# Kernel tuning notes

Hardware: AMD Instinct MI355X
Metric: run time of the kernel (lower is better)

Reference implementation:

```python
import jax, jax.numpy as jnp
import numpy as np

N_NODES = 100000


def gcn_conv(x, edge_index, W, b, num_nodes):
    """PyG GCNConv: y = D^{-1/2} (A + I) D^{-1/2} (x W) + b.

    edge_index[0] = source (row), edge_index[1] = target (col);
    messages flow source -> target with symmetric normalization.
    """
    # add self loops
    loop = jnp.arange(num_nodes, dtype=edge_index.dtype)
    row = jnp.concatenate([edge_index[0], loop])  # [E+N]
    col = jnp.concatenate([edge_index[1], loop])  # [E+N]

    xw = x @ W  # [N, F_out] -- tiny GEMM, done before gather

    # degree of target nodes (incl. self loops)
    ones = jnp.ones(col.shape[0], dtype=x.dtype)
    deg = jax.ops.segment_sum(ones, col, num_segments=num_nodes)  # [N]
    dis = jax.lax.rsqrt(jnp.maximum(deg, 1e-12))
    dis = jnp.where(deg > 0, dis, 0.0)

    norm = dis[row] * dis[col]  # [E+N]
    msg = xw[row] * norm[:, None]  # gather + scale, [E+N, F_out]
    out = jax.ops.segment_sum(msg, col, num_segments=num_nodes)  # scatter-add
    return out + b


def setup_inputs() -> dict:
    key = jax.random.key(0)
    k1, k2, k3, k4 = jax.random.split(key, 4)
    num_attr, hidden, num_classes = 128, 16, 8
    n_edges = 3200000
    x = jax.random.normal(k1, (N_NODES, num_attr), dtype=jnp.float32)
    edge_index = jax.random.randint(k2, (2, n_edges), 0, N_NODES, dtype=jnp.int64)
    W1 = jax.random.normal(k3, (num_attr, hidden), dtype=jnp.float32) / np.sqrt(num_attr)
    b1 = jnp.zeros((hidden,), dtype=jnp.float32)
    W2 = jax.random.normal(k4, (hidden, num_classes), dtype=jnp.float32) / np.sqrt(hidden)
    b2 = jnp.zeros((num_classes,), dtype=jnp.float32)
    return {"x": x, "edge_index": edge_index, "W1": W1, "b1": b1, "W2": W2, "b2": b2}


def reference(x, edge_index, W1, b1, W2, b2):
    h = gcn_conv(x, edge_index, W1, b1, N_NODES)
    h = jax.nn.relu(h)
    # dropout is identity in eval mode
    h = gcn_conv(h, edge_index, W2, b2, N_NODES)
    return jax.nn.sigmoid(h)  # [N, num_classes]
```

## Files before the change

### kernel.cpp

```cpp
#include <hip/hip_runtime.h>
#include <math.h>

static constexpr int FI = 128;
static constexpr int FH = 16;
static constexpr int FO = 8;

static constexpr int BIN_SHIFT = 8;
static constexpr int BIN_NODES = 256;
static constexpr int MAX_BINS  = 512;
static constexpr int CAPB      = 8832;
static constexpr int SCHUNK    = 8192;
static constexpr int SThreads  = 512;

__device__ __forceinline__ unsigned short f2bf(float x) {
    unsigned u = __float_as_uint(x);
    u += 0x7FFFu + ((u >> 16) & 1u);
    return (unsigned short)(u >> 16);
}
__device__ __forceinline__ float bflo(unsigned u) { return __uint_as_float(u << 16); }
__device__ __forceinline__ float bfhi(unsigned u) { return __uint_as_float(u & 0xFFFF0000u); }

__global__ void k_initcur(int* __restrict__ binCursor, int nbins) {
    int i = blockIdx.x * 256 + threadIdx.x;
    if (i < nbins) binCursor[i] = i * CAPB;
}

__launch_bounds__(SThreads)
__global__ void k_binscatter(const int* __restrict__ row, const int* __restrict__ col,
                             int* __restrict__ binCursor, unsigned int* __restrict__ binned,
                             int E, int nbins) {
    __shared__ int lcnt[MAX_BINS];
    __shared__ int lsc[MAX_BINS];
    __shared__ int lstart[MAX_BINS];
    __shared__ int lcur[MAX_BINS];
    __shared__ int gbase[MAX_BINS];
    __shared__ unsigned int   staged[SCHUNK];
    __shared__ unsigned short sbin[SCHUNK];
    int t = threadIdx.x;
    int base = blockIdx.x * SCHUNK;
    int end  = base + SCHUNK; if (end > E) end = E;
    int m = end - base;
    if (t < MAX_BINS) lcnt[t] = 0;
    __syncthreads();

    int nv = m >> 2;
    const int4* c4 = (const int4*)(col + base);
    for (int k = t; k < nv; k += SThreads) {
        int4 c = c4[k];
        atomicAdd(&lcnt[c.x >> BIN_SHIFT], 1);
        atomicAdd(&lcnt[c.y >> BIN_SHIFT], 1);
        atomicAdd(&lcnt[c.z >> BIN_SHIFT], 1);
        atomicAdd(&lcnt[c.w >> BIN_SHIFT], 1);
    }
    for (int i = base + (nv << 2) + t; i < end; i += SThreads)
        atomicAdd(&lcnt[col[i] >> BIN_SHIFT], 1);
    __syncthreads();

    int v = 0;
    if (t < MAX_BINS) { v = lcnt[t]; lsc[t] = v; }
    __syncthreads();
    for (int off = 1; off < MAX_BINS; off <<= 1) {
        int x = (t >= off && t < MAX_BINS) ? lsc[t - off] : 0;
        __syncthreads();
        if (t < MAX_BINS) lsc[t] += x;
        __syncthreads();
    }
    if (t < MAX_BINS) {
        int ex = lsc[t] - v;
        lstart[t] = ex;
        lcur[t]   = ex;
        gbase[t]  = v ? atomicAdd(&binCursor[t], v) : 0;
    }
    __syncthreads();

    const int4* r4 = (const int4*)(row + base);
    for (int k = t; k < nv; k += SThreads) {
        int4 c = c4[k]; int4 r = r4[k];
        int cc[4] = {c.x, c.y, c.z, c.w};
        int rr[4] = {r.x, r.y, r.z, r.w};
        #pragma unroll
        for (int j = 0; j < 4; ++j) {
            int b = cc[j] >> BIN_SHIFT;
            int pos = atomicAdd(&lcur[b], 1);
            staged[pos] = (unsigned)rr[j] | ((unsigned)(cc[j] & (BIN_NODES - 1)) << 17);
            sbin[pos] = (unsigned short)b;
        }
    }
    for (int i = base + (nv << 2) + t; i < end; i += SThreads) {
        int c = col[i];
        int b = c >> BIN_SHIFT;
        int pos = atomicAdd(&lcur[b], 1);
        staged[pos] = (unsigned)row[i] | ((unsigned)(c & (BIN_NODES - 1)) << 17);
        sbin[pos] = (unsigned short)b;
    }
    __syncthreads();

    for (int i = t; i < m; i += SThreads) {
        int b = sbin[i];
        int g = gbase[b] + (i - lstart[b]);
        if (g < (b + 1) * CAPB) binned[g] = staged[i];
    }
}

__launch_bounds__(BIN_NODES)
__global__ void k_refine(const int* __restrict__ binCursor, const unsigned int* __restrict__ binned,
                         int* __restrict__ srow, int* __restrict__ starts, int* __restrict__ ends,
                         float* __restrict__ dis, int N) {
    __shared__ int cnt[BIN_NODES];
    __shared__ int wsum[4];
    int t = threadIdx.x;
    int b = blockIdx.x;
    int s = b * CAPB;
    int m = binCursor[b] - s;
    if (m > CAPB) m = CAPB;
    cnt[t] = 0;
    __syncthreads();

    int mm = m & ~3;
    for (int i0 = t * 4; i0 < mm; i0 += BIN_NODES * 4) {
        uint4 v = *(const uint4*)(binned + s + i0);
        atomicAdd(&cnt[v.x >> 17], 1);
        atomicAdd(&cnt[v.y >> 17], 1);
        atomicAdd(&cnt[v.z >> 17], 1);
        atomicAdd(&cnt[v.w >> 17], 1);
    }
    for (int i = mm + t; i < m; i += BIN_NODES)
        atomicAdd(&cnt[binned[s + i] >> 17], 1);
    __syncthreads();

    int deg = cnt[t];
    int inc = deg;
    #pragma unroll
    for (int d = 1; d < 64; d <<= 1) {
        int u = __shfl_up(inc, d, 64);
        if ((t & 63) >= d) inc += u;
    }
    if ((t & 63) == 63) wsum[t >> 6] = inc;
    __syncthreads();
    if (t < 4) {
        int w = wsum[t];
        #pragma unroll
        for (int d = 1; d < 4; d <<= 1) {
            int u = __shfl_up(w, d, 4);
            if (t >= d) w += u;
        }
        wsum[t] = w;
    }
    __syncthreads();
    int waveoff = (t >= 64) ? wsum[(t >> 6) - 1] : 0;
    int excl = waveoff + inc - deg;

    int n = b * BIN_NODES + t;
    if (n < N) {
        starts[n] = s + excl;
        ends[n]   = s + excl + deg;
        dis[n]    = rsqrtf((float)(deg + 1));
    }
    cnt[t] = excl;
    __syncthreads();

    for (int i0 = t * 4; i0 < mm; i0 += BIN_NODES * 4) {
        uint4 v = *(const uint4*)(binned + s + i0);
        int p0 = atomicAdd(&cnt[v.x >> 17], 1); srow[s + p0] = v.x & 0x1FFFF;
        int p1 = atomicAdd(&cnt[v.y >> 17], 1); srow[s + p1] = v.y & 0x1FFFF;
        int p2 = atomicAdd(&cnt[v.z >> 17], 1); srow[s + p2] = v.z & 0x1FFFF;
        int p3 = atomicAdd(&cnt[v.w >> 17], 1); srow[s + p3] = v.w & 0x1FFFF;
    }
    for (int i = mm + t; i < m; i += BIN_NODES) {
        unsigned v = binned[s + i];
        int p = atomicAdd(&cnt[v >> 17], 1);
        srow[s + p] = v & 0x1FFFF;
    }
}

__launch_bounds__(256)
__global__ void k_gemm1(const float* __restrict__ x, const float* __restrict__ W,
                        const float* __restrict__ dis, unsigned short* __restrict__ xw1s,
                        int N) {
    __shared__ float sw[FI * FH];
    int t = threadIdx.x;
    for (int i = t; i < FI * FH; i += 256) sw[i] = W[i];
    __syncthreads();

    int nl = t >> 2;
    int f  = (t & 3) * 4;
    int n  = blockIdx.x * 64 + nl;
    if (n >= N) return;

    const float4* xr = (const float4*)(x + (size_t)n * FI);
    float a0 = 0.f, a1 = 0.f, a2 = 0.f, a3 = 0.f;
    #pragma unroll 8
    for (int kq = 0; kq < FI / 4; ++kq) {
        float4 xv = xr[kq];
        float4 w0 = *(const float4*)&sw[(kq * 4 + 0) * FH + f];
        float4 w1 = *(const float4*)&sw[(kq * 4 + 1) * FH + f];
        float4 w2 = *(const float4*)&sw[(kq * 4 + 2) * FH + f];
        float4 w3 = *(const float4*)&sw[(kq * 4 + 3) * FH + f];
        a0 = fmaf(xv.x, w0.x, a0); a1 = fmaf(xv.x, w0.y, a1);
        a2 = fmaf(xv.x, w0.z, a2); a3 = fmaf(xv.x, w0.w, a3);
        a0 = fmaf(xv.y, w1.x, a0); a1 = fmaf(xv.y, w1.y, a1);
        a2 = fmaf(xv.y, w1.z, a2); a3 = fmaf(xv.y, w1.w, a3);
        a0 = fmaf(xv.z, w2.x, a0); a1 = fmaf(xv.z, w2.y, a1);
        a2 = fmaf(xv.z, w2.z, a2); a3 = fmaf(xv.z, w2.w, a3);
        a0 = fmaf(xv.w, w3.x, a0); a1 = fmaf(xv.w, w3.y, a1);
        a2 = fmaf(xv.w, w3.z, a2); a3 = fmaf(xv.w, w3.w, a3);
    }
    float dn = dis[n];
    unsigned w0 = (unsigned)f2bf(a0 * dn) | ((unsigned)f2bf(a1 * dn) << 16);
    unsigned w1 = (unsigned)f2bf(a2 * dn) | ((unsigned)f2bf(a3 * dn) << 16);
    *(uint2*)(xw1s + (size_t)n * FH + f) = make_uint2(w0, w1);
}

__launch_bounds__(128)
__global__ void k_agg1(const int* __restrict__ starts, const int* __restrict__ ends,
                       const int* __restrict__ srow, const float* __restrict__ dis,
                       const unsigned short* __restrict__ xw1s, const float* __restrict__ W2,
                       const float* __restrict__ b1, unsigned short* __restrict__ xw2s, int N) {
    __shared__ float sw[FH * FO];
    __shared__ float sb[FH];
    int t = threadIdx.x;
    if (t < FH * FO) sw[t] = W2[t];
    if (t < FH) sb[t] = b1[t];
    __syncthreads();

    int n = blockIdx.x * 128 + t;
    if (n >= N) return;
    float dn = dis[n];
    int s = starts[n], e = ends[n];
    const uint4* xq = (const uint4*)xw1s;

    uint4 s0 = xq[(size_t)n * 2], s1 = xq[(size_t)n * 2 + 1];
    float acc[16];
    acc[0]=bflo(s0.x); acc[1]=bfhi(s0.x); acc[2]=bflo(s0.y); acc[3]=bfhi(s0.y);
    acc[4]=bflo(s0.z); acc[5]=bfhi(s0.z); acc[6]=bflo(s0.w); acc[7]=bfhi(s0.w);
    acc[8]=bflo(s1.x); acc[9]=bfhi(s1.x); acc[10]=bflo(s1.y); acc[11]=bfhi(s1.y);
    acc[12]=bflo(s1.z); acc[13]=bfhi(s1.z); acc[14]=bflo(s1.w); acc[15]=bfhi(s1.w);

    int i = s;
    for (; i + 8 <= e; i += 8) {
        int rr[8];
        #pragma unroll
        for (int j = 0; j < 8; ++j) rr[j] = srow[i + j];
        uint4 pa[8], pb[8];
        #pragma unroll
        for (int j = 0; j < 8; ++j) {
            pa[j] = xq[(size_t)rr[j] * 2];
            pb[j] = xq[(size_t)rr[j] * 2 + 1];
        }
        #pragma unroll
        for (int j = 0; j < 8; ++j) {
            acc[0]+=bflo(pa[j].x);  acc[1]+=bfhi(pa[j].x);
            acc[2]+=bflo(pa[j].y);  acc[3]+=bfhi(pa[j].y);
            acc[4]+=bflo(pa[j].z);  acc[5]+=bfhi(pa[j].z);
            acc[6]+=bflo(pa[j].w);  acc[7]+=bfhi(pa[j].w);
            acc[8]+=bflo(pb[j].x);  acc[9]+=bfhi(pb[j].x);
            acc[10]+=bflo(pb[j].y); acc[11]+=bfhi(pb[j].y);
            acc[12]+=bflo(pb[j].z); acc[13]+=bfhi(pb[j].z);
            acc[14]+=bflo(pb[j].w); acc[15]+=bfhi(pb[j].w);
        }
    }
    for (; i < e; ++i) {
        int r = srow[i];
        uint4 qa = xq[(size_t)r * 2], qb = xq[(size_t)r * 2 + 1];
        acc[0]+=bflo(qa.x);  acc[1]+=bfhi(qa.x);
        acc[2]+=bflo(qa.y);  acc[3]+=bfhi(qa.y);
        acc[4]+=bflo(qa.z);  acc[5]+=bfhi(qa.z);
        acc[6]+=bflo(qa.w);  acc[7]+=bfhi(qa.w);
        acc[8]+=bflo(qb.x);  acc[9]+=bfhi(qb.x);
        acc[10]+=bflo(qb.y); acc[11]+=bfhi(qb.y);
        acc[12]+=bflo(qb.z); acc[13]+=bfhi(qb.z);
        acc[14]+=bflo(qb.w); acc[15]+=bfhi(qb.w);
    }

    float hv[FH];
    #pragma unroll
    for (int k = 0; k < FH; ++k) {
        float v = fmaf(dn, acc[k], sb[k]);
        hv[k] = v > 0.f ? v : 0.f;
    }
    unsigned o[4];
    #pragma unroll
    for (int p = 0; p < 4; ++p) {
        float aL = 0.f, aH = 0.f;
        #pragma unroll
        for (int k = 0; k < FH; ++k) {
            aL = fmaf(hv[k], sw[k * FO + 2 * p],     aL);
            aH = fmaf(hv[k], sw[k * FO + 2 * p + 1], aH);
        }
        o[p] = (unsigned)f2bf(aL * dn) | ((unsigned)f2bf(aH * dn) << 16);
    }
    *(uint4*)(xw2s + (size_t)n * FO) = make_uint4(o[0], o[1], o[2], o[3]);
}

__launch_bounds__(128)
__global__ void k_agg2(const int* __restrict__ starts, const int* __restrict__ ends,
                       const int* __restrict__ srow, const float* __restrict__ dis,
                       const unsigned short* __restrict__ xw2s, const float* __restrict__ b2,
                       float* __restrict__ out, int N) {
    int t = threadIdx.x;
    int n = blockIdx.x * 128 + t;
    if (n >= N) return;
    float dn = dis[n];
    int s = starts[n], e = ends[n];
    const uint4* xq = (const uint4*)xw2s;

    uint4 sp = xq[n];
    float acc[8];
    acc[0]=bflo(sp.x); acc[1]=bfhi(sp.x); acc[2]=bflo(sp.y); acc[3]=bfhi(sp.y);
    acc[4]=bflo(sp.z); acc[5]=bfhi(sp.z); acc[6]=bflo(sp.w); acc[7]=bfhi(sp.w);

    int i = s;
    for (; i + 8 <= e; i += 8) {
        int rr[8];
        #pragma unroll
        for (int j = 0; j < 8; ++j) rr[j] = srow[i + j];
        uint4 pk[8];
        #pragma unroll
        for (int j = 0; j < 8; ++j) pk[j] = xq[rr[j]];
        #pragma unroll
        for (int j = 0; j < 8; ++j) {
            acc[0]+=bflo(pk[j].x); acc[1]+=bfhi(pk[j].x);
            acc[2]+=bflo(pk[j].y); acc[3]+=bfhi(pk[j].y);
            acc[4]+=bflo(pk[j].z); acc[5]+=bfhi(pk[j].z);
            acc[6]+=bflo(pk[j].w); acc[7]+=bfhi(pk[j].w);
        }
    }
    for (; i < e; ++i) {
        uint4 p = xq[srow[i]];
        acc[0]+=bflo(p.x); acc[1]+=bfhi(p.x);
        acc[2]+=bflo(p.y); acc[3]+=bfhi(p.y);
        acc[4]+=bflo(p.z); acc[5]+=bfhi(p.z);
        acc[6]+=bflo(p.w); acc[7]+=bfhi(p.w);
    }

    float r[FO];
    #pragma unroll
    for (int k = 0; k < FO; ++k) {
        float v = fmaf(dn, acc[k], b2[k]);
        r[k] = 1.f / (1.f + __expf(-v));
    }
    *(float4*)(out + (size_t)n * FO)     = make_float4(r[0], r[1], r[2], r[3]);
    *(float4*)(out + (size_t)n * FO + 4) = make_float4(r[4], r[5], r[6], r[7]);
}

extern "C" void kernel_launch(void* const* d_in, const int* in_sizes, int n_in,
                              void* d_out, int out_size, void* d_ws, size_t ws_size,
                              hipStream_t stream) {
    const float* x  = (const float*)d_in[0];
    const int*   ei = (const int*)d_in[1];
    const float* W1 = (const float*)d_in[2];
    const float* b1 = (const float*)d_in[3];
    const float* W2 = (const float*)d_in[4];
    const float* b2 = (const float*)d_in[5];

    const int N = in_sizes[0] / FI;
    const int E = in_sizes[1] / 2;
    const int* row = ei;
    const int* col = ei + E;
    const int nbins = (N + BIN_NODES - 1) >> BIN_SHIFT;

    const size_t NP = 100352;
    const size_t BINSZ = (size_t)nbins * CAPB;
    float* base = (float*)d_ws;
    int*   starts    = (int*)base;
    int*   ends      = (int*)(base + NP);
    float* dis       = base + 2 * NP;
    int*   binCursor = (int*)(base + 3 * NP);
    unsigned int* binned = (unsigned int*)(base + 3 * NP + 1024);
    int*   srow      = (int*)(base + 3 * NP + 1024 + BINSZ);
    unsigned short* xw1s = (unsigned short*)binned;
    unsigned short* xw2s = (unsigned short*)(base + 3 * NP + 1024 + NP * 8);
    float* out = (float*)d_out;

    size_t needed = (3 * NP + 1024 + 2 * BINSZ) * 4;
    if (ws_size < needed) return;

    k_initcur   <<<(nbins + 255) / 256, 256,             0, stream>>>(binCursor, nbins);
    k_binscatter<<<(E + SCHUNK - 1) / SCHUNK, SThreads,  0, stream>>>(row, col, binCursor, binned, E, nbins);
    k_refine    <<<nbins, BIN_NODES,                     0, stream>>>(binCursor, binned, srow, starts, ends, dis, N);
    k_gemm1     <<<(N + 63) / 64, 256,                   0, stream>>>(x, W1, dis, xw1s, N);
    k_agg1      <<<(N + 127) / 128, 128,                 0, stream>>>(starts, ends, srow, dis, xw1s, W2, b1, xw2s, N);
    k_agg2      <<<(N + 127) / 128, 128,                 0, stream>>>(starts, ends, srow, dis, xw2s, b2, out, N);
}
```

Measured before the change: 125.1 us.

## Fuse GEMM1 into refine kernel, split agg features across thread pairs, cache col in registers

```diff
diff --git a/kernel.cpp b/kernel.cpp
--- a/kernel.cpp
+++ b/kernel.cpp
@@ -45,12 +45,17 @@
 
     int nv = m >> 2;
     const int4* c4 = (const int4*)(col + base);
-    for (int k = t; k < nv; k += SThreads) {
-        int4 c = c4[k];
-        atomicAdd(&lcnt[c.x >> BIN_SHIFT], 1);
-        atomicAdd(&lcnt[c.y >> BIN_SHIFT], 1);
-        atomicAdd(&lcnt[c.z >> BIN_SHIFT], 1);
-        atomicAdd(&lcnt[c.w >> BIN_SHIFT], 1);
+    int4 creg[4];
+    #pragma unroll
+    for (int j = 0; j < 4; ++j) {
+        int k = t + j * SThreads;
+        if (k < nv) {
+            creg[j] = c4[k];
+            atomicAdd(&lcnt[creg[j].x >> BIN_SHIFT], 1);
+            atomicAdd(&lcnt[creg[j].y >> BIN_SHIFT], 1);
+            atomicAdd(&lcnt[creg[j].z >> BIN_SHIFT], 1);
+            atomicAdd(&lcnt[creg[j].w >> BIN_SHIFT], 1);
+        }
     }
     for (int i = base + (nv << 2) + t; i < end; i += SThreads)
         atomicAdd(&lcnt[col[i] >> BIN_SHIFT], 1);
@@ -74,16 +79,20 @@
     __syncthreads();
 
     const int4* r4 = (const int4*)(row + base);
-    for (int k = t; k < nv; k += SThreads) {
-        int4 c = c4[k]; int4 r = r4[k];
-        int cc[4] = {c.x, c.y, c.z, c.w};
-        int rr[4] = {r.x, r.y, r.z, r.w};
-        #pragma unroll
-        for (int j = 0; j < 4; ++j) {
-            int b = cc[j] >> BIN_SHIFT;
-            int pos = atomicAdd(&lcur[b], 1);
-            staged[pos] = (unsigned)rr[j] | ((unsigned)(cc[j] & (BIN_NODES - 1)) << 17);
-            sbin[pos] = (unsigned short)b;
+    #pragma unroll
+    for (int j = 0; j < 4; ++j) {
+        int k = t + j * SThreads;
+        if (k < nv) {
+            int4 r = r4[k];
+            int cc[4] = {creg[j].x, creg[j].y, creg[j].z, creg[j].w};
+            int rr[4] = {r.x, r.y, r.z, r.w};
+            #pragma unroll
+            for (int jj = 0; jj < 4; ++jj) {
+                int b = cc[jj] >> BIN_SHIFT;
+                int pos = atomicAdd(&lcur[b], 1);
+                staged[pos] = (unsigned)rr[jj] | ((unsigned)(cc[jj] & (BIN_NODES - 1)) << 17);
+                sbin[pos] = (unsigned short)b;
+            }
         }
     }
     for (int i = base + (nv << 2) + t; i < end; i += SThreads) {
@@ -102,18 +111,23 @@
     }
 }
 
-__launch_bounds__(BIN_NODES)
-__global__ void k_refine(const int* __restrict__ binCursor, const unsigned int* __restrict__ binned,
-                         int* __restrict__ srow, int* __restrict__ starts, int* __restrict__ ends,
-                         float* __restrict__ dis, int N) {
+__launch_bounds__(256)
+__global__ void k_refine_gemm(const int* __restrict__ binCursor, const unsigned int* __restrict__ binned,
+                              int* __restrict__ srow, int* __restrict__ starts, int* __restrict__ ends,
+                              float* __restrict__ dis, const float* __restrict__ x,
+                              const float* __restrict__ W1, unsigned short* __restrict__ xw1s, int N) {
     __shared__ int cnt[BIN_NODES];
     __shared__ int wsum[4];
+    __shared__ float sdis[BIN_NODES];
+    __shared__ float sw[FI * FH];
+    __shared__ float sx[64 * 132];
     int t = threadIdx.x;
     int b = blockIdx.x;
     int s = b * CAPB;
     int m = binCursor[b] - s;
     if (m > CAPB) m = CAPB;
     cnt[t] = 0;
+    for (int i = t; i < FI * FH; i += 256) sw[i] = W1[i];
     __syncthreads();
 
     int mm = m & ~3;
@@ -151,11 +165,13 @@
     int excl = waveoff + inc - deg;
 
     int n = b * BIN_NODES + t;
+    float dv = rsqrtf((float)(deg + 1));
     if (n < N) {
         starts[n] = s + excl;
         ends[n]   = s + excl + deg;
-        dis[n]    = rsqrtf((float)(deg + 1));
-    }
+        dis[n]    = dv;
+    }
+    sdis[t] = dv;
     cnt[t] = excl;
     __syncthreads();
 
@@ -171,47 +187,43 @@
         int p = atomicAdd(&cnt[v >> 17], 1);
         srow[s + p] = v & 0x1FFFF;
     }
-}
-
-__launch_bounds__(256)
-__global__ void k_gemm1(const float* __restrict__ x, const float* __restrict__ W,
-                        const float* __restrict__ dis, unsigned short* __restrict__ xw1s,
-                        int N) {
-    __shared__ float sw[FI * FH];
-    int t = threadIdx.x;
-    for (int i = t; i < FI * FH; i += 256) sw[i] = W[i];
-    __syncthreads();
 
     int nl = t >> 2;
     int f  = (t & 3) * 4;
-    int n  = blockIdx.x * 64 + nl;
-    if (n >= N) return;
-
-    const float4* xr = (const float4*)(x + (size_t)n * FI);
-    float a0 = 0.f, a1 = 0.f, a2 = 0.f, a3 = 0.f;
-    #pragma unroll 8
-    for (int kq = 0; kq < FI / 4; ++kq) {
-        float4 xv = xr[kq];
-        float4 w0 = *(const float4*)&sw[(kq * 4 + 0) * FH + f];
-        float4 w1 = *(const float4*)&sw[(kq * 4 + 1) * FH + f];
-        float4 w2 = *(const float4*)&sw[(kq * 4 + 2) * FH + f];
-        float4 w3 = *(const float4*)&sw[(kq * 4 + 3) * FH + f];
-        a0 = fmaf(xv.x, w0.x, a0); a1 = fmaf(xv.x, w0.y, a1);
-        a2 = fmaf(xv.x, w0.z, a2); a3 = fmaf(xv.x, w0.w, a3);
-        a0 = fmaf(xv.y, w1.x, a0); a1 = fmaf(xv.y, w1.y, a1);
-        a2 = fmaf(xv.y, w1.z, a2); a3 = fmaf(xv.y, w1.w, a3);
-        a0 = fmaf(xv.z, w2.x, a0); a1 = fmaf(xv.z, w2.y, a1);
-        a2 = fmaf(xv.z, w2.z, a2); a3 = fmaf(xv.z, w2.w, a3);
-        a0 = fmaf(xv.w, w3.x, a0); a1 = fmaf(xv.w, w3.y, a1);
-        a2 = fmaf(xv.w, w3.z, a2); a3 = fmaf(xv.w, w3.w, a3);
-    }
-    float dn = dis[n];
-    unsigned w0 = (unsigned)f2bf(a0 * dn) | ((unsigned)f2bf(a1 * dn) << 16);
-    unsigned w1 = (unsigned)f2bf(a2 * dn) | ((unsigned)f2bf(a3 * dn) << 16);
-    *(uint2*)(xw1s + (size_t)n * FH + f) = make_uint2(w0, w1);
-}
-
-__launch_bounds__(128)
+    for (int c = 0; c < 4; ++c) {
+        __syncthreads();
+        int rbase = b * BIN_NODES + c * 64;
+        int rows = N - rbase;
+        rows = rows < 0 ? 0 : (rows > 64 ? 64 : rows);
+        const float4* xg = (const float4*)(x + (size_t)rbase * FI);
+        for (int i = t; i < rows * 32; i += 256) {
+            int r = i >> 5, cc = i & 31;
+            float4 vv = xg[(size_t)r * 32 + cc];
+            float* dst = &sx[r * 132 + cc * 4];
+            dst[0] = vv.x; dst[1] = vv.y; dst[2] = vv.z; dst[3] = vv.w;
+        }
+        __syncthreads();
+        int nn = rbase + nl;
+        if (nn < N) {
+            float a0 = 0.f, a1 = 0.f, a2 = 0.f, a3 = 0.f;
+            #pragma unroll 4
+            for (int k = 0; k < FI; k++) {
+                float xv = sx[nl * 132 + k];
+                const float* wr = &sw[k * FH + f];
+                a0 = fmaf(xv, wr[0], a0);
+                a1 = fmaf(xv, wr[1], a1);
+                a2 = fmaf(xv, wr[2], a2);
+                a3 = fmaf(xv, wr[3], a3);
+            }
+            float dn = sdis[c * 64 + nl];
+            unsigned w0 = (unsigned)f2bf(a0 * dn) | ((unsigned)f2bf(a1 * dn) << 16);
+            unsigned w1 = (unsigned)f2bf(a2 * dn) | ((unsigned)f2bf(a3 * dn) << 16);
+            *(uint2*)(xw1s + (size_t)nn * FH + f) = make_uint2(w0, w1);
+        }
+    }
+}
+
+__launch_bounds__(256)
 __global__ void k_agg1(const int* __restrict__ starts, const int* __restrict__ ends,
                        const int* __restrict__ srow, const float* __restrict__ dis,
                        const unsigned short* __restrict__ xw1s, const float* __restrict__ W2,
@@ -223,124 +235,109 @@
     if (t < FH) sb[t] = b1[t];
     __syncthreads();
 
-    int n = blockIdx.x * 128 + t;
+    int n = blockIdx.x * 128 + (t >> 1);
+    int h = t & 1;
     if (n >= N) return;
     float dn = dis[n];
     int s = starts[n], e = ends[n];
     const uint4* xq = (const uint4*)xw1s;
 
-    uint4 s0 = xq[(size_t)n * 2], s1 = xq[(size_t)n * 2 + 1];
-    float acc[16];
-    acc[0]=bflo(s0.x); acc[1]=bfhi(s0.x); acc[2]=bflo(s0.y); acc[3]=bfhi(s0.y);
-    acc[4]=bflo(s0.z); acc[5]=bfhi(s0.z); acc[6]=bflo(s0.w); acc[7]=bfhi(s0.w);
-    acc[8]=bflo(s1.x); acc[9]=bfhi(s1.x); acc[10]=bflo(s1.y); acc[11]=bfhi(s1.y);
-    acc[12]=bflo(s1.z); acc[13]=bfhi(s1.z); acc[14]=bflo(s1.w); acc[15]=bfhi(s1.w);
+    uint4 sp = xq[(size_t)n * 2 + h];
+    float acc[8];
+    acc[0]=bflo(sp.x); acc[1]=bfhi(sp.x); acc[2]=bflo(sp.y); acc[3]=bfhi(sp.y);
+    acc[4]=bflo(sp.z); acc[5]=bfhi(sp.z); acc[6]=bflo(sp.w); acc[7]=bfhi(sp.w);
 
     int i = s;
     for (; i + 8 <= e; i += 8) {
         int rr[8];
         #pragma unroll
         for (int j = 0; j < 8; ++j) rr[j] = srow[i + j];
-        uint4 pa[8], pb[8];
+        uint4 pk[8];
+        #pragma unroll
+        for (int j = 0; j < 8; ++j) pk[j] = xq[(size_t)rr[j] * 2 + h];
         #pragma unroll
         for (int j = 0; j < 8; ++j) {
-            pa[j] = xq[(size_t)rr[j] * 2];
-            pb[j] = xq[(size_t)rr[j] * 2 + 1];
-        }
-        #pragma unroll
-        for (int j = 0; j < 8; ++j) {
-            acc[0]+=bflo(pa[j].x);  acc[1]+=bfhi(pa[j].x);
-            acc[2]+=bflo(pa[j].y);  acc[3]+=bfhi(pa[j].y);
-            acc[4]+=bflo(pa[j].z);  acc[5]+=bfhi(pa[j].z);
-            acc[6]+=bflo(pa[j].w);  acc[7]+=bfhi(pa[j].w);
-            acc[8]+=bflo(pb[j].x);  acc[9]+=bfhi(pb[j].x);
-            acc[10]+=bflo(pb[j].y); acc[11]+=bfhi(pb[j].y);
-            acc[12]+=bflo(pb[j].z); acc[13]+=bfhi(pb[j].z);
-            acc[14]+=bflo(pb[j].w); acc[15]+=bfhi(pb[j].w);
+            acc[0]+=bflo(pk[j].x); acc[1]+=bfhi(pk[j].x);
+            acc[2]+=bflo(pk[j].y); acc[3]+=bfhi(pk[j].y);
+            acc[4]+=bflo(pk[j].z); acc[5]+=bfhi(pk[j].z);
+            acc[6]+=bflo(pk[j].w); acc[7]+=bfhi(pk[j].w);
         }
     }
     for (; i < e; ++i) {
-        int r = srow[i];
-        uint4 qa = xq[(size_t)r * 2], qb = xq[(size_t)r * 2 + 1];
-        acc[0]+=bflo(qa.x);  acc[1]+=bfhi(qa.x);
-        acc[2]+=bflo(qa.y);  acc[3]+=bfhi(qa.y);
-        acc[4]+=bflo(qa.z);  acc[5]+=bfhi(qa.z);
-        acc[6]+=bflo(qa.w);  acc[7]+=bfhi(qa.w);
-        acc[8]+=bflo(qb.x);  acc[9]+=bfhi(qb.x);
-        acc[10]+=bflo(qb.y); acc[11]+=bfhi(qb.y);
-        acc[12]+=bflo(qb.z); acc[13]+=bfhi(qb.z);
-        acc[14]+=bflo(qb.w); acc[15]+=bfhi(qb.w);
-    }
-
-    float hv[FH];
-    #pragma unroll
-    for (int k = 0; k < FH; ++k) {
-        float v = fmaf(dn, acc[k], sb[k]);
+        uint4 p = xq[(size_t)srow[i] * 2 + h];
+        acc[0]+=bflo(p.x); acc[1]+=bfhi(p.x);
+        acc[2]+=bflo(p.y); acc[3]+=bfhi(p.y);
+        acc[4]+=bflo(p.z); acc[5]+=bfhi(p.z);
+        acc[6]+=bflo(p.w); acc[7]+=bfhi(p.w);
+    }
+
+    float hv[8];
+    #pragma unroll
+    for (int k = 0; k < 8; ++k) {
+        float v = fmaf(dn, acc[k], sb[h * 8 + k]);
         hv[k] = v > 0.f ? v : 0.f;
     }
-    unsigned o[4];
-    #pragma unroll
-    for (int p = 0; p < 4; ++p) {
-        float aL = 0.f, aH = 0.f;
-        #pragma unroll
-        for (int k = 0; k < FH; ++k) {
-            aL = fmaf(hv[k], sw[k * FO + 2 * p],     aL);
-            aH = fmaf(hv[k], sw[k * FO + 2 * p + 1], aH);
-        }
-        o[p] = (unsigned)f2bf(aL * dn) | ((unsigned)f2bf(aH * dn) << 16);
-    }
-    *(uint4*)(xw2s + (size_t)n * FO) = make_uint4(o[0], o[1], o[2], o[3]);
-}
-
-__launch_bounds__(128)
+    float po[FO];
+    #pragma unroll
+    for (int o = 0; o < FO; ++o) {
+        float a = 0.f;
+        #pragma unroll
+        for (int k = 0; k < 8; ++k) a = fmaf(hv[k], sw[(h * 8 + k) * FO + o], a);
+        po[o] = a;
+    }
+    #pragma unroll
+    for (int o = 0; o < FO; ++o) po[o] += __shfl_xor(po[o], 1, 64);
+    int o0 = h * 4;
+    unsigned w0 = (unsigned)f2bf(po[o0 + 0] * dn) | ((unsigned)f2bf(po[o0 + 1] * dn) << 16);
+    unsigned w1 = (unsigned)f2bf(po[o0 + 2] * dn) | ((unsigned)f2bf(po[o0 + 3] * dn) << 16);
+    *(uint2*)(xw2s + (size_t)n * FO + o0) = make_uint2(w0, w1);
+}
+
+__launch_bounds__(256)
 __global__ void k_agg2(const int* __restrict__ starts, const int* __restrict__ ends,
                        const int* __restrict__ srow, const float* __restrict__ dis,
                        const unsigned short* __restrict__ xw2s, const float* __restrict__ b2,
                        float* __restrict__ out, int N) {
     int t = threadIdx.x;
-    int n = blockIdx.x * 128 + t;
+    int n = blockIdx.x * 128 + (t >> 1);
+    int h = t & 1;
     if (n >= N) return;
     float dn = dis[n];
     int s = starts[n], e = ends[n];
-    const uint4* xq = (const uint4*)xw2s;
-
-    uint4 sp = xq[n];
-    float acc[8];
+    const uint2* xq = (const uint2*)xw2s;
+
+    uint2 sp = xq[(size_t)n * 2 + h];
+    float acc[4];
     acc[0]=bflo(sp.x); acc[1]=bfhi(sp.x); acc[2]=bflo(sp.y); acc[3]=bfhi(sp.y);
-    acc[4]=bflo(sp.z); acc[5]=bfhi(sp.z); acc[6]=bflo(sp.w); acc[7]=bfhi(sp.w);
 
     int i = s;
     for (; i + 8 <= e; i += 8) {
         int rr[8];
         #pragma unroll
         for (int j = 0; j < 8; ++j) rr[j] = srow[i + j];
-        uint4 pk[8];
-        #pragma unroll
-        for (int j = 0; j < 8; ++j) pk[j] = xq[rr[j]];
+        uint2 pk[8];
+        #pragma unroll
+        for (int j = 0; j < 8; ++j) pk[j] = xq[(size_t)rr[j] * 2 + h];
         #pragma unroll
         for (int j = 0; j < 8; ++j) {
             acc[0]+=bflo(pk[j].x); acc[1]+=bfhi(pk[j].x);
             acc[2]+=bflo(pk[j].y); acc[3]+=bfhi(pk[j].y);
-            acc[4]+=bflo(pk[j].z); acc[5]+=bfhi(pk[j].z);
-            acc[6]+=bflo(pk[j].w); acc[7]+=bfhi(pk[j].w);
         }
     }
     for (; i < e; ++i) {
-        uint4 p = xq[srow[i]];
+        uint2 p = xq[(size_t)srow[i] * 2 + h];
         acc[0]+=bflo(p.x); acc[1]+=bfhi(p.x);
         acc[2]+=bflo(p.y); acc[3]+=bfhi(p.y);
-        acc[4]+=bflo(p.z); acc[5]+=bfhi(p.z);
-        acc[6]+=bflo(p.w); acc[7]+=bfhi(p.w);
-    }
-
-    float r[FO];
-    #pragma unroll
-    for (int k = 0; k < FO; ++k) {
-        float v = fmaf(dn, acc[k], b2[k]);
+    }
+
+    int f0 = h * 4;
+    float r[4];
+    #pragma unroll
+    for (int k = 0; k < 4; ++k) {
+        float v = fmaf(dn, acc[k], b2[f0 + k]);
         r[k] = 1.f / (1.f + __expf(-v));
     }
-    *(float4*)(out + (size_t)n * FO)     = make_float4(r[0], r[1], r[2], r[3]);
-    *(float4*)(out + (size_t)n * FO + 4) = make_float4(r[4], r[5], r[6], r[7]);
+    *(float4*)(out + (size_t)n * FO + f0) = make_float4(r[0], r[1], r[2], r[3]);
 }
 
 extern "C" void kernel_launch(void* const* d_in, const int* in_sizes, int n_in,
@@ -368,17 +365,16 @@
     int*   binCursor = (int*)(base + 3 * NP);
     unsigned int* binned = (unsigned int*)(base + 3 * NP + 1024);
     int*   srow      = (int*)(base + 3 * NP + 1024 + BINSZ);
-    unsigned short* xw1s = (unsigned short*)binned;
-    unsigned short* xw2s = (unsigned short*)(base + 3 * NP + 1024 + NP * 8);
+    unsigned short* xw1s = (unsigned short*)(base + 3 * NP + 1024 + 2 * BINSZ);
+    unsigned short* xw2s = (unsigned short*)(base + 3 * NP + 1024 + 2 * BINSZ + NP * 8);
     float* out = (float*)d_out;
 
-    size_t needed = (3 * NP + 1024 + 2 * BINSZ) * 4;
+    size_t needed = (3 * NP + 1024 + 2 * BINSZ + NP * 12) * 4;
     if (ws_size < needed) return;
 
-    k_initcur   <<<(nbins + 255) / 256, 256,             0, stream>>>(binCursor, nbins);
-    k_binscatter<<<(E + SCHUNK - 1) / SCHUNK, SThreads,  0, stream>>>(row, col, binCursor, binned, E, nbins);
-    k_refine    <<<nbins, BIN_NODES,                     0, stream>>>(binCursor, binned, srow, starts, ends, dis, N);
-    k_gemm1     <<<(N + 63) / 64, 256,                   0, stream>>>(x, W1, dis, xw1s, N);
-    k_agg1      <<<(N + 127) / 128, 128,                 0, stream>>>(starts, ends, srow, dis, xw1s, W2, b1, xw2s, N);
-    k_agg2      <<<(N + 127) / 128, 128,                 0, stream>>>(starts, ends, srow, dis, xw2s, b2, out, N);
-}
+    k_initcur    <<<(nbins + 255) / 256, 256,             0, stream>>>(binCursor, nbins);
+    k_binscatter <<<(E + SCHUNK - 1) / SCHUNK, SThreads,  0, stream>>>(row, col, binCursor, binned, E, nbins);
+    k_refine_gemm<<<nbins, BIN_NODES,                     0, stream>>>(binCursor, binned, srow, starts, ends, dis, x, W1, xw1s, N);
+    k_agg1       <<<(2 * N + 255) / 256, 256,             0, stream>>>(starts, ends, srow, dis, xw1s, W2, b1, xw2s, N);
+    k_agg2       <<<(2 * N + 255) / 256, 256,             0, stream>>>(starts, ends, srow, dis, xw2s, b2, out, N);
+}
```

After: 125.9 us (median of 3 runs). No clear change (+0.7%).
